# Performance work log

Measured on AMD Instinct MI355X. Metric: run time of the kernel, lower is better.

Reference implementation:

```python
import jax, jax.numpy as jnp
import numpy as np
import math

D, H, L, V, F, B, S = 1024, 16, 4, 32000, 4096, 1, 2048
HD = D // H
LN_EPS = 1e-5


def _alibi_slopes(n_heads):
    # power-of-2 case from the torch code
    start = 2.0 ** (-2.0 ** (-(math.log2(n_heads) - 3)))
    return np.array([start * (start ** i) for i in range(n_heads)], dtype=np.float32)


def setup_inputs() -> dict:
    key = jax.random.key(0)
    ks = jax.random.split(key, 10)
    sc = 0.02
    return {
        "input_ids": jax.random.randint(ks[0], (B, S), 0, V, dtype=jnp.int64 if jax.config.jax_enable_x64 else jnp.int32),
        "emb": jax.random.normal(ks[1], (V, D), jnp.float32) * sc,
        "alibi_slopes": jnp.asarray(_alibi_slopes(H)),
        "Wq": jax.random.normal(ks[2], (L, D, D), jnp.float32) * sc,
        "Wk": jax.random.normal(ks[3], (L, D, D), jnp.float32) * sc,
        "Wv": jax.random.normal(ks[4], (L, D, D), jnp.float32) * sc,
        "Wo": jax.random.normal(ks[5], (L, D, D), jnp.float32) * sc,
        "W1": jax.random.normal(ks[6], (L, F, D), jnp.float32) * sc,
        "b1": jnp.zeros((L, F), jnp.float32),
        "W2": jax.random.normal(ks[7], (L, D, F), jnp.float32) * sc,
        "b2": jnp.zeros((L, D), jnp.float32),
        "g1": jnp.ones((L, D), jnp.float32),
        "beta1": jnp.zeros((L, D), jnp.float32),
        "g2": jnp.ones((L, D), jnp.float32),
        "beta2": jnp.zeros((L, D), jnp.float32),
        "gf": jnp.ones((D,), jnp.float32),
        "bf": jnp.zeros((D,), jnp.float32),
    }


def _layernorm(x, g, b):
    m = jnp.mean(x, axis=-1, keepdims=True)
    v = jnp.var(x, axis=-1, keepdims=True)
    return (x - m) * jax.lax.rsqrt(v + LN_EPS) * g + b


def _forward(input_ids, emb, alibi_slopes, Wq, Wk, Wv, Wo, W1, b1, W2, b2,
             g1, beta1, g2, beta2, gf, bf):
    x = emb[input_ids]  # [B, S, D]
    pos = jnp.arange(S, dtype=jnp.float32)
    dist = pos[None, :] - pos[:, None]          # [S, S], entry (i, j) = j - i
    causal = dist <= 0                           # tril mask
    bias = alibi_slopes[None, :, None, None] * dist  # [1, H, S, S]
    scale = 1.0 / math.sqrt(HD)

    def layer(x, p):
        wq, wk, wv, wo, w1, bb1, w2, bb2, gg1, be1, gg2, be2 = p
        h = _layernorm(x, gg1, be1)
        q = jnp.einsum('bsd,ed->bse', h, wq).reshape(B, S, H, HD).transpose(0, 2, 1, 3)
        k = jnp.einsum('bsd,ed->bse', h, wk).reshape(B, S, H, HD).transpose(0, 2, 1, 3)
        v = jnp.einsum('bsd,ed->bse', h, wv).reshape(B, S, H, HD).transpose(0, 2, 1, 3)
        scores = jnp.einsum('bhqd,bhkd->bhqk', q, k) * scale
        scores = scores - bias
        scores = jnp.where(causal, scores, -jnp.inf)
        w = jax.nn.softmax(scores, axis=-1)
        out = jnp.einsum('bhqk,bhkd->bhqd', w, v)
        out = out.transpose(0, 2, 1, 3).reshape(B, S, D)
        out = jnp.einsum('bsd,ed->bse', out, wo)
        x = x + out
        h2 = _layernorm(x, gg2, be2)
        ff = jax.nn.gelu(jnp.einsum('bsd,fd->bsf', h2, w1) + bb1, approximate=False)
        ff = jnp.einsum('bsf,df->bsd', ff, w2) + bb2
        return x + ff, None

    params = (Wq, Wk, Wv, Wo, W1, b1, W2, b2, g1, beta1, g2, beta2)
    x, _ = jax.lax.scan(layer, x, params)
    x = _layernorm(x, gf, bf)
    logits = jnp.einsum('bsd,vd->bsv', x, emb)  # tied lm_head
    return logits


def reference(input_ids, emb, alibi_slopes, Wq, Wk, Wv, Wo, W1, b1, W2, b2,
              g1, beta1, g2, beta2, gf, bf):
    return _forward(input_ids, emb, alibi_slopes, Wq, Wk, Wv, Wo, W1, b1, W2, b2,
                    g1, beta1, g2, beta2, gf, bf)
```

## Files before the change

kernel.cpp:

```cpp
#include <hip/hip_runtime.h>
#include <hip/hip_bf16.h>

typedef unsigned int u32;
typedef unsigned short u16;
typedef __attribute__((ext_vector_type(8))) __bf16 bf16x8;
typedef __attribute__((ext_vector_type(8))) unsigned short u16x8;
typedef __attribute__((ext_vector_type(4))) float f32x4;

#define SEQ 2048

__device__ __forceinline__ float b2f(u16 u) {
  union { u32 i; float f; } x; x.i = ((u32)u) << 16; return x.f;
}
__device__ __forceinline__ u16 f2b(float f) {
  u32 u = __float_as_uint(f);
  u = (u + 0x7fffu + ((u >> 16) & 1u)) >> 16;
  return (u16)u;
}
__device__ __forceinline__ void gload_lds16(const void* g, void* l) {
  __builtin_amdgcn_global_load_lds((const __attribute__((address_space(1))) u32*)g,
                                   (__attribute__((address_space(3))) u32*)l, 16, 0, 0);
}

struct CvtArgs {
  const float* src[7];
  u16* dst[7];
  u32 beg[8];
  u32 total;
};

__global__ __launch_bounds__(256) void cvt_all(CvtArgs a)
{
  for (u32 i = blockIdx.x * 256 + threadIdx.x; i < a.total; i += gridDim.x * 256) {
    int s = 0;
#pragma unroll
    for (int k = 1; k < 7; ++k) s += (i >= a.beg[k]);
    const u32 li = i - a.beg[s];
    const float* in = a.src[s];
    const float4 f0 = ((const float4*)in)[(size_t)li * 2];
    const float4 f1 = ((const float4*)in)[(size_t)li * 2 + 1];
    union { bf16x8 b; u16x8 u; } r;
    r.b[0] = (__bf16)f0.x; r.b[1] = (__bf16)f0.y;
    r.b[2] = (__bf16)f0.z; r.b[3] = (__bf16)f0.w;
    r.b[4] = (__bf16)f1.x; r.b[5] = (__bf16)f1.y;
    r.b[6] = (__bf16)f1.z; r.b[7] = (__bf16)f1.w;
    *(u16x8*)(a.dst[s] + (size_t)li * 8) = r.u;
  }
}

template <int EPI>
__global__ __launch_bounds__(256) void gemm_bt64(
    const u16* __restrict__ A, const u16* __restrict__ Bt,
    void* __restrict__ C0, int N, int K)
{
  __shared__ u16 As[128 * 64];
  __shared__ u16 Bs[128 * 64];
  const int tid = threadIdx.x;
  const int lane = tid & 63;
  const int w = tid >> 6;
  const int wr = w >> 1;
  const int wc = w & 1;

  const int T = (int)gridDim.x;
  const int bid = (int)blockIdx.x;
  const int q8 = T >> 3, r8 = T & 7;
  const int xcd = bid & 7, base = bid >> 3;
  int swz = (xcd < r8 ? xcd * (q8 + 1) : r8 * (q8 + 1) + (xcd - r8) * q8) + base;
  const int m0 = (swz & 15) * 128;
  const int n0 = (swz >> 4) * 128;

  f32x4 acc[4][4] = {};

  const int rs = lane >> 3;
  const int gs = (lane & 7) ^ rs;
  const u16* ga0 = A + (size_t)(m0 + w * 32 + rs) * K + gs * 8;
  const u16* gb0 = Bt + (size_t)(n0 + w * 32 + rs) * K + gs * 8;
  u16* la = &As[(w * 32) * 64];
  u16* lb = &Bs[(w * 32) * 64];

  const int xg = lane & 7;
  int coff[2];
#pragma unroll
  for (int ks = 0; ks < 2; ++ks)
    coff[ks] = ((ks * 4 + (lane >> 4)) ^ xg) * 8;
  const int ra = (wr * 64 + (lane & 15)) * 64;
  const int rb = (wc * 64 + (lane & 15)) * 64;

  for (int kt = 0; kt < K; kt += 64) {
    __syncthreads();
#pragma unroll
    for (int c = 0; c < 4; ++c) {
      gload_lds16(ga0 + (size_t)c * 8 * K + kt, la + c * 8 * 64);
      gload_lds16(gb0 + (size_t)c * 8 * K + kt, lb + c * 8 * 64);
    }
    asm volatile("s_waitcnt vmcnt(0)" ::: "memory");
    __syncthreads();
#pragma unroll
    for (int ks = 0; ks < 2; ++ks) {
      bf16x8 af[4], bfr[4];
#pragma unroll
      for (int m = 0; m < 4; ++m)
        af[m] = *(const bf16x8*)&As[ra + m * 16 * 64 + coff[ks]];
#pragma unroll
      for (int n = 0; n < 4; ++n)
        bfr[n] = *(const bf16x8*)&Bs[rb + n * 16 * 64 + coff[ks]];
#pragma unroll
      for (int m = 0; m < 4; ++m)
#pragma unroll
        for (int n = 0; n < 4; ++n)
          acc[m][n] = __builtin_amdgcn_mfma_f32_16x16x32_bf16(af[m], bfr[n], acc[m][n], 0, 0, 0);
    }
  }

#pragma unroll
  for (int m = 0; m < 4; ++m) {
    const int rowb = m0 + wr * 64 + m * 16 + ((lane >> 4) << 2);
#pragma unroll
    for (int n = 0; n < 4; ++n) {
      const int col = n0 + wc * 64 + n * 16 + (lane & 15);
#pragma unroll
      for (int j = 0; j < 4; ++j)
        ((float*)C0)[(size_t)(rowb + j) * N + col] = acc[m][n][j];
    }
  }
}

template <int EPI>
__global__ __launch_bounds__(256) void gemm64(
    const u16* __restrict__ A, const u16* __restrict__ B0,
    const u16* __restrict__ B1, const u16* __restrict__ B2,
    void* __restrict__ C0, void* __restrict__ C1, void* __restrict__ C2,
    const float* __restrict__ bias, int N, int K)
{
  __shared__ u16 As[64 * 64];
  __shared__ u16 Bs[128 * 64];
  const int tid = threadIdx.x;
  const int lane = tid & 63;
  const int w = tid >> 6;
  const int wr = w >> 1;
  const int wc = w & 1;

  const int T = (int)gridDim.x;
  const int bid = (int)blockIdx.x;
  const int q8 = T >> 3, r8 = T & 7;
  const int xcd = bid & 7, base = bid >> 3;
  int swz = (xcd < r8 ? xcd * (q8 + 1) : r8 * (q8 + 1) + (xcd - r8) * q8) + base;
  int which = 0;
  if (EPI == 1) which = swz >> 8;
  const u16* Bt = (which == 0) ? B0 : (which == 1) ? B1 : B2;
  const int m0 = (swz & 31) * 64;
  const int n0 = (EPI == 1 ? ((swz >> 5) & 7) : (swz >> 5)) * 128;

  const int kchunk = K / (int)gridDim.z;
  const int kbeg = (int)blockIdx.z * kchunk;
  const int kend = kbeg + kchunk;

  f32x4 acc[2][4] = {};

  const int rs = lane >> 3;
  const int gs = (lane & 7) ^ rs;
  const u16* ga0 = A + (size_t)(m0 + w * 16 + rs) * K + gs * 8;
  const u16* gb0 = Bt + (size_t)(n0 + w * 32 + rs) * K + gs * 8;
  u16* la = &As[(w * 16) * 64];
  u16* lb = &Bs[(w * 32) * 64];

  const int xg = lane & 7;
  int coff[2];
#pragma unroll
  for (int ks = 0; ks < 2; ++ks)
    coff[ks] = ((ks * 4 + (lane >> 4)) ^ xg) * 8;
  const int ra = (wr * 32 + (lane & 15)) * 64;
  const int rb = (wc * 64 + (lane & 15)) * 64;

  for (int kt = kbeg; kt < kend; kt += 64) {
    __syncthreads();
#pragma unroll
    for (int c = 0; c < 2; ++c)
      gload_lds16(ga0 + (size_t)c * 8 * K + kt, la + c * 8 * 64);
#pragma unroll
    for (int c = 0; c < 4; ++c)
      gload_lds16(gb0 + (size_t)c * 8 * K + kt, lb + c * 8 * 64);
    asm volatile("s_waitcnt vmcnt(0)" ::: "memory");
    __syncthreads();
#pragma unroll
    for (int ks = 0; ks < 2; ++ks) {
      bf16x8 af[2], bfr[4];
#pragma unroll
      for (int m = 0; m < 2; ++m)
        af[m] = *(const bf16x8*)&As[ra + m * 16 * 64 + coff[ks]];
#pragma unroll
      for (int n = 0; n < 4; ++n)
        bfr[n] = *(const bf16x8*)&Bs[rb + n * 16 * 64 + coff[ks]];
#pragma unroll
      for (int m = 0; m < 2; ++m)
#pragma unroll
        for (int n = 0; n < 4; ++n)
          acc[m][n] = __builtin_amdgcn_mfma_f32_16x16x32_bf16(af[m], bfr[n], acc[m][n], 0, 0, 0);
    }
  }

#pragma unroll
  for (int m = 0; m < 2; ++m) {
    const int rowb = m0 + wr * 32 + m * 16 + ((lane >> 4) << 2);
#pragma unroll
    for (int n = 0; n < 4; ++n) {
      const int col = n0 + wc * 64 + n * 16 + (lane & 15);
#pragma unroll
      for (int j = 0; j < 4; ++j) {
        const int r = rowb + j;
        float v = acc[m][n][j];
        if (EPI == 1) {
          u16* outp = (u16*)((which == 0) ? C0 : (which == 1) ? C1 : C2);
          outp[((size_t)(col >> 6) * SEQ + r) * 64 + (col & 63)] = f2b(v);
        } else if (EPI == 2) {
          float xx = v + bias[col];
          float ge = 0.5f * xx * (1.0f + erff(xx * 0.70710678118654752f));
          ((u16*)C0)[(size_t)r * N + col] = f2b(ge);
        } else {
          float xx = v;
          if (bias != nullptr && blockIdx.z == 0) xx += bias[col];
          atomicAdd(&((float*)C0)[(size_t)r * N + col], xx);
        }
      }
    }
  }
}

__global__ __launch_bounds__(256) void gemm_f32b(
    const u16* __restrict__ A, const float* __restrict__ Bt,
    float* __restrict__ C0, int N, int K)
{
  __shared__ u16 As[128 * 32];
  __shared__ u16 Bs[128 * 32];
  const int tid = threadIdx.x;
  const int lane = tid & 63;
  const int w = tid >> 6;
  const int wr = w >> 1;
  const int wc = w & 1;

  const int T = (int)gridDim.x;
  const int bid = (int)blockIdx.x;
  const int q8 = T >> 3, r8 = T & 7;
  const int xcd = bid & 7, base = bid >> 3;
  int swz = (xcd < r8 ? xcd * (q8 + 1) : r8 * (q8 + 1) + (xcd - r8) * q8) + base;
  const int m0 = (swz & 15) * 128;
  const int n0 = (swz >> 4) * 128;

  f32x4 acc[4][4] = {};
  const u16* ga0 = A + (size_t)(m0 + w * 32 + (lane >> 2)) * K + (lane & 3) * 8;
  u16* la = &As[(w * 32) * 32];
  const float* gb32 = Bt + (size_t)(n0 + (tid >> 1)) * K + (tid & 1) * 16;
  u16* lbw = &Bs[(tid >> 1) * 32 + (tid & 1) * 16];

  for (int kt = 0; kt < K; kt += 32) {
    __syncthreads();
    gload_lds16(ga0 + kt, la);
    gload_lds16(ga0 + kt + 16 * K, la + 16 * 32);
    {
      const float4 f0 = *(const float4*)(gb32 + kt);
      const float4 f1 = *(const float4*)(gb32 + kt + 4);
      const float4 f2 = *(const float4*)(gb32 + kt + 8);
      const float4 f3 = *(const float4*)(gb32 + kt + 12);
      union { bf16x8 b; u16x8 u; } lo, hi;
      lo.b[0] = (__bf16)f0.x; lo.b[1] = (__bf16)f0.y;
      lo.b[2] = (__bf16)f0.z; lo.b[3] = (__bf16)f0.w;
      lo.b[4] = (__bf16)f1.x; lo.b[5] = (__bf16)f1.y;
      lo.b[6] = (__bf16)f1.z; lo.b[7] = (__bf16)f1.w;
      hi.b[0] = (__bf16)f2.x; hi.b[1] = (__bf16)f2.y;
      hi.b[2] = (__bf16)f2.z; hi.b[3] = (__bf16)f2.w;
      hi.b[4] = (__bf16)f3.x; hi.b[5] = (__bf16)f3.y;
      hi.b[6] = (__bf16)f3.z; hi.b[7] = (__bf16)f3.w;
      *(u16x8*)lbw = lo.u;
      *(u16x8*)(lbw + 8) = hi.u;
    }
    asm volatile("s_waitcnt vmcnt(0)" ::: "memory");
    __syncthreads();
    bf16x8 af[4], bfr[4];
#pragma unroll
    for (int m = 0; m < 4; ++m)
      af[m] = *(const bf16x8*)&As[(wr * 64 + m * 16 + (lane & 15)) * 32 + (lane >> 4) * 8];
#pragma unroll
    for (int n = 0; n < 4; ++n)
      bfr[n] = *(const bf16x8*)&Bs[(wc * 64 + n * 16 + (lane & 15)) * 32 + (lane >> 4) * 8];
#pragma unroll
    for (int m = 0; m < 4; ++m)
#pragma unroll
      for (int n = 0; n < 4; ++n)
        acc[m][n] = __builtin_amdgcn_mfma_f32_16x16x32_bf16(af[m], bfr[n], acc[m][n], 0, 0, 0);
  }

#pragma unroll
  for (int m = 0; m < 4; ++m) {
    const int rowb = m0 + wr * 64 + m * 16 + ((lane >> 4) << 2);
#pragma unroll
    for (int n = 0; n < 4; ++n) {
      const int col = n0 + wc * 64 + n * 16 + (lane & 15);
#pragma unroll
      for (int j = 0; j < 4; ++j)
        C0[(size_t)(rowb + j) * N + col] = acc[m][n][j];
    }
  }
}

__global__ __launch_bounds__(256) void ln_kernel(const float* __restrict__ x,
    const float* __restrict__ g, const float* __restrict__ b, u16* __restrict__ out)
{
  const int row = blockIdx.x;
  const int tid = threadIdx.x;
  const float4 v = ((const float4*)(x + (size_t)row * 1024))[tid];
  float s = v.x + v.y + v.z + v.w;
  float sq = v.x * v.x + v.y * v.y + v.z * v.z + v.w * v.w;
#pragma unroll
  for (int o = 1; o < 64; o <<= 1) { s += __shfl_xor(s, o); sq += __shfl_xor(sq, o); }
  __shared__ float ss[4], ssq[4];
  if ((tid & 63) == 0) { ss[tid >> 6] = s; ssq[tid >> 6] = sq; }
  __syncthreads();
  s = ss[0] + ss[1] + ss[2] + ss[3];
  sq = ssq[0] + ssq[1] + ssq[2] + ssq[3];
  const float mean = s * (1.0f / 1024.0f);
  const float var = sq * (1.0f / 1024.0f) - mean * mean;
  const float rstd = rsqrtf(var + 1e-5f);
  const int c = tid * 4;
  u16* o4 = out + (size_t)row * 1024 + c;
  const float4 gg = ((const float4*)g)[tid];
  const float4 bb = ((const float4*)b)[tid];
  o4[0] = f2b((v.x - mean) * rstd * gg.x + bb.x);
  o4[1] = f2b((v.y - mean) * rstd * gg.y + bb.y);
  o4[2] = f2b((v.z - mean) * rstd * gg.z + bb.z);
  o4[3] = f2b((v.w - mean) * rstd * gg.w + bb.w);
}

__global__ __launch_bounds__(256) void gather_kernel(const int* __restrict__ ids,
    const float* __restrict__ emb, float* __restrict__ x)
{
  const int srow = blockIdx.x;
  const int tid = threadIdx.x;
  const int id = ids[srow];
  ((float4*)(x + (size_t)srow * 1024))[tid] =
      ((const float4*)(emb + (size_t)id * 1024))[tid];
}

__global__ __launch_bounds__(256) void attn_kernel(
    const u16* __restrict__ q, const u16* __restrict__ k, const u16* __restrict__ v,
    const float* __restrict__ slopes, u16* __restrict__ out)
{
  const int bid = (int)blockIdx.x;
  const int swz = (bid & 7) * 32 + (bid >> 3);
  const int h = swz >> 4;
  const int q0 = (swz & 15) * 128;
  const int tid = threadIdx.x;
  const int lane = tid & 63;
  const int w = tid >> 6;
  const float slope = slopes[h];

  __shared__ u16 Ks[2][64 * 32];
  __shared__ u16 Vt[64][72];
  __shared__ u16 Pl[4][32][72];

  const u16* qb = q + ((size_t)h * SEQ + q0 + w * 32) * 64;
  bf16x8 qf[2][2];
#pragma unroll
  for (int m = 0; m < 2; ++m)
#pragma unroll
    for (int kk = 0; kk < 2; ++kk)
      qf[m][kk] = *(const bf16x8*)(qb + (m * 16 + (lane & 15)) * 64 + kk * 32 + (lane >> 4) * 8);

  f32x4 o_acc[2][4] = {};
  float mrun[2][4], lrun[2][4];
#pragma unroll
  for (int m = 0; m < 2; ++m)
#pragma unroll
    for (int j = 0; j < 4; ++j) { mrun[m][j] = -1e30f; lrun[m][j] = 0.0f; }

  const int ntiles = (q0 >> 6) + 2;
  const int wmaxrow = q0 + w * 32 + 31;

  const int kkp = w >> 1, halfp = w & 1;
  const u16* gk0 = k + ((size_t)h * SEQ + halfp * 32 + (lane >> 2)) * 64 + kkp * 32 + (lane & 3) * 8;
  u16* lk = &Ks[kkp][(halfp * 32) * 32];
  const u16* gv0 = v + ((size_t)h * SEQ + lane) * 64 + w * 16;

  for (int t = 0; t < ntiles; ++t) {
    const int j0 = t << 6;
    __syncthreads();
    gload_lds16(gk0 + (size_t)j0 * 64, lk);
    gload_lds16(gk0 + (size_t)(j0 + 16) * 64, lk + 16 * 32);
    {
      const u16* gvp = gv0 + (size_t)j0 * 64;
      u16x8 v0 = *(const u16x8*)gvp;
      u16x8 v1 = *(const u16x8*)(gvp + 8);
      const int d0 = w * 16;
#pragma unroll
      for (int i = 0; i < 8; ++i) Vt[d0 + i][lane] = v0[i];
#pragma unroll
      for (int i = 0; i < 8; ++i) Vt[d0 + 8 + i][lane] = v1[i];
    }
    asm volatile("s_waitcnt vmcnt(0)" ::: "memory");
    __syncthreads();

    if (wmaxrow >= j0) {
      f32x4 s[2][4] = {};
      __builtin_amdgcn_s_setprio(1);
#pragma unroll
      for (int kk = 0; kk < 2; ++kk) {
        bf16x8 kf[4];
#pragma unroll
        for (int n = 0; n < 4; ++n)
          kf[n] = *(const bf16x8*)&Ks[kk][(n * 16 + (lane & 15)) * 32 + (lane >> 4) * 8];
#pragma unroll
        for (int m = 0; m < 2; ++m)
#pragma unroll
          for (int n = 0; n < 4; ++n)
            s[m][n] = __builtin_amdgcn_mfma_f32_16x16x32_bf16(qf[m][kk], kf[n], s[m][n], 0, 0, 0);
      }
      __builtin_amdgcn_s_setprio(0);
      const int rq = q0 + w * 32 + ((lane >> 4) << 2);
      const int ck = j0 + (lane & 15);
#pragma unroll
      for (int m = 0; m < 2; ++m) {
#pragma unroll
        for (int j = 0; j < 4; ++j) {
          const int qi = rq + m * 16 + j;
          float mx = -1e30f;
#pragma unroll
          for (int n = 0; n < 4; ++n) {
            const int kj = ck + n * 16;
            float val = s[m][n][j] * 0.125f - slope * (float)(kj - qi);
            val = (kj <= qi) ? val : -1e30f;
            s[m][n][j] = val;
            mx = fmaxf(mx, val);
          }
#pragma unroll
          for (int o = 1; o < 16; o <<= 1) mx = fmaxf(mx, __shfl_xor(mx, o));
          const float mnew = fmaxf(mrun[m][j], mx);
          const float alpha = __expf(mrun[m][j] - mnew);
          mrun[m][j] = mnew;
          float rs = 0.0f;
          const int prow = m * 16 + ((lane >> 4) << 2) + j;
#pragma unroll
          for (int n = 0; n < 4; ++n) {
            const float p = __expf(s[m][n][j] - mnew);
            rs += p;
            Pl[w][prow][n * 16 + (lane & 15)] = f2b(p);
          }
#pragma unroll
          for (int o = 1; o < 16; o <<= 1) rs += __shfl_xor(rs, o);
          lrun[m][j] = lrun[m][j] * alpha + rs;
#pragma unroll
          for (int n = 0; n < 4; ++n) o_acc[m][n][j] *= alpha;
        }
      }
      __builtin_amdgcn_s_setprio(1);
#pragma unroll
      for (int kk = 0; kk < 2; ++kk) {
        bf16x8 pf[2], vf[4];
#pragma unroll
        for (int m = 0; m < 2; ++m)
          pf[m] = *(const bf16x8*)&Pl[w][m * 16 + (lane & 15)][kk * 32 + (lane >> 4) * 8];
#pragma unroll
        for (int n = 0; n < 4; ++n)
          vf[n] = *(const bf16x8*)&Vt[n * 16 + (lane & 15)][kk * 32 + (lane >> 4) * 8];
#pragma unroll
        for (int m = 0; m < 2; ++m)
#pragma unroll
          for (int n = 0; n < 4; ++n)
            o_acc[m][n] = __builtin_amdgcn_mfma_f32_16x16x32_bf16(pf[m], vf[n], o_acc[m][n], 0, 0, 0);
      }
      __builtin_amdgcn_s_setprio(0);
    }
  }

#pragma unroll
  for (int m = 0; m < 2; ++m) {
    const int sbase = q0 + w * 32 + m * 16 + ((lane >> 4) << 2);
#pragma unroll
    for (int n = 0; n < 4; ++n) {
      const int d = h * 64 + n * 16 + (lane & 15);
#pragma unroll
      for (int j = 0; j < 4; ++j)
        out[(size_t)(sbase + j) * 1024 + d] = f2b(o_acc[m][n][j] / lrun[m][j]);
    }
  }
}

extern "C" void kernel_launch(void* const* d_in, const int* in_sizes, int n_in,
                              void* d_out, int out_size, void* d_ws, size_t ws_size,
                              hipStream_t stream)
{
  (void)in_sizes; (void)n_in; (void)out_size;
  const int* ids = (const int*)d_in[0];
  const float* emb = (const float*)d_in[1];
  const float* slopes = (const float*)d_in[2];
  const float* Wq = (const float*)d_in[3];
  const float* Wk = (const float*)d_in[4];
  const float* Wv = (const float*)d_in[5];
  const float* Wo = (const float*)d_in[6];
  const float* W1 = (const float*)d_in[7];
  const float* b1 = (const float*)d_in[8];
  const float* W2 = (const float*)d_in[9];
  const float* b2 = (const float*)d_in[10];
  const float* g1 = (const float*)d_in[11];
  const float* be1 = (const float*)d_in[12];
  const float* g2 = (const float*)d_in[13];
  const float* be2 = (const float*)d_in[14];
  const float* gf = (const float*)d_in[15];
  const float* bfin = (const float*)d_in[16];

  char* ob = (char*)d_out;
  float* x   = (float*)ob;
  u16* qb    = (u16*)(ob + (size_t)( 8u << 20));
  u16* kb    = (u16*)(ob + (size_t)(12u << 20));
  u16* vb    = (u16*)(ob + (size_t)(16u << 20));
  u16* attn  = (u16*)(ob + (size_t)(20u << 20));
  u16* ff    = (u16*)(ob + (size_t)(24u << 20));
  u16* Wq_b  = (u16*)(ob + (size_t)( 40u << 20));
  u16* Wk_b  = (u16*)(ob + (size_t)( 48u << 20));
  u16* Wv_b  = (u16*)(ob + (size_t)( 56u << 20));
  u16* Wo_b  = (u16*)(ob + (size_t)( 64u << 20));
  u16* W1_b  = (u16*)(ob + (size_t)( 72u << 20));
  u16* W2_b  = (u16*)(ob + (size_t)(104u << 20));
  u16* h     = (u16*)d_ws;
  const size_t emb_b_need = (size_t)(4u << 20) + (size_t)32000 * 1024 * 2;
  const bool emb_fits = ws_size >= emb_b_need;
  u16* emb_b = (u16*)((char*)d_ws + (4u << 20));
  float* logits = (float*)d_out;

  {
    CvtArgs a;
    const u32 wsz = 4 * 1024 * 1024 / 8;
    const u32 fsz = 16 * 1024 * 1024 / 8;
    const u32 esz = 32000 * 1024 / 8;
    a.src[0] = Wq; a.dst[0] = Wq_b;
    a.src[1] = Wk; a.dst[1] = Wk_b;
    a.src[2] = Wv; a.dst[2] = Wv_b;
    a.src[3] = Wo; a.dst[3] = Wo_b;
    a.src[4] = W1; a.dst[4] = W1_b;
    a.src[5] = W2; a.dst[5] = W2_b;
    a.src[6] = emb; a.dst[6] = emb_b;
    a.beg[0] = 0;
    a.beg[1] = wsz;      a.beg[2] = 2 * wsz;  a.beg[3] = 3 * wsz;
    a.beg[4] = 4 * wsz;  a.beg[5] = 4 * wsz + fsz;  a.beg[6] = 4 * wsz + 2 * fsz;
    a.beg[7] = a.beg[6] + esz;
    a.total = emb_fits ? a.beg[7] : a.beg[6];
    cvt_all<<<2048, 256, 0, stream>>>(a);
  }

  gather_kernel<<<2048, 256, 0, stream>>>(ids, emb, x);

  for (int l = 0; l < 4; ++l) {
    const size_t wo = (size_t)l * 1024 * 1024;
    const size_t wf = (size_t)l * 4096 * 1024;
    ln_kernel<<<2048, 256, 0, stream>>>(x, g1 + l * 1024, be1 + l * 1024, h);
    gemm64<1><<<dim3(768, 1, 1), 256, 0, stream>>>(h, Wq_b + wo, Wk_b + wo, Wv_b + wo,
        qb, kb, vb, nullptr, 1024, 1024);
    attn_kernel<<<dim3(256, 1, 1), 256, 0, stream>>>(qb, kb, vb, slopes, attn);
    gemm64<3><<<dim3(256, 1, 2), 256, 0, stream>>>(attn, Wo_b + wo, nullptr, nullptr,
        x, nullptr, nullptr, nullptr, 1024, 1024);
    ln_kernel<<<2048, 256, 0, stream>>>(x, g2 + l * 1024, be2 + l * 1024, h);
    gemm64<2><<<dim3(1024, 1, 1), 256, 0, stream>>>(h, W1_b + wf, nullptr, nullptr,
        ff, nullptr, nullptr, b1 + l * 4096, 4096, 1024);
    gemm64<3><<<dim3(256, 1, 2), 256, 0, stream>>>(ff, W2_b + wf, nullptr, nullptr,
        x, nullptr, nullptr, b2 + l * 1024, 1024, 4096);
  }
  ln_kernel<<<2048, 256, 0, stream>>>(x, gf, bfin, h);
  if (emb_fits) {
    gemm_bt64<0><<<dim3(4000, 1, 1), 256, 0, stream>>>(h, emb_b, logits, 32000, 1024);
  } else {
    gemm_f32b<<<dim3(4000, 1, 1), 256, 0, stream>>>(h, emb, logits, 32000, 1024);
  }
}
```

Before: 1.353 ms.

## Replace lm_head GEMM with 256x256 double-buffered 8-wave kernel

Swaps the 128x128 single-buffered logits GEMM for a 256x256-tile kernel with 512 threads, double-buffered LDS and next-tile global-to-LDS loads interleaved with MFMA phases, plus setprio around the MFMA bursts. The aim is higher arithmetic intensity per tile and hiding global load latency behind compute in the largest GEMM (2048x32000x1024). The cost is 128KB of LDS per block and more accumulator registers, which limits occupancy, and a grid of 1000 blocks that leaves a tail imbalance across CUs.

```diff
diff --git a/kernel.cpp b/kernel.cpp
--- a/kernel.cpp
+++ b/kernel.cpp
@@ -48,81 +48,109 @@
   }
 }
 
-template <int EPI>
-__global__ __launch_bounds__(256) void gemm_bt64(
+__global__ __launch_bounds__(512, 2) void gemm256(
     const u16* __restrict__ A, const u16* __restrict__ Bt,
-    void* __restrict__ C0, int N, int K)
-{
-  __shared__ u16 As[128 * 64];
-  __shared__ u16 Bs[128 * 64];
+    float* __restrict__ C, int N, int K)
+{
+  __shared__ u16 As[2][256 * 64];
+  __shared__ u16 Bs[2][256 * 64];
   const int tid = threadIdx.x;
   const int lane = tid & 63;
-  const int w = tid >> 6;
-  const int wr = w >> 1;
-  const int wc = w & 1;
+  const int wid = tid >> 6;
+  const int wr = wid >> 2;
+  const int wc = wid & 3;
 
   const int T = (int)gridDim.x;
   const int bid = (int)blockIdx.x;
   const int q8 = T >> 3, r8 = T & 7;
   const int xcd = bid & 7, base = bid >> 3;
-  int swz = (xcd < r8 ? xcd * (q8 + 1) : r8 * (q8 + 1) + (xcd - r8) * q8) + base;
-  const int m0 = (swz & 15) * 128;
-  const int n0 = (swz >> 4) * 128;
-
-  f32x4 acc[4][4] = {};
-
-  const int rs = lane >> 3;
-  const int gs = (lane & 7) ^ rs;
-  const u16* ga0 = A + (size_t)(m0 + w * 32 + rs) * K + gs * 8;
-  const u16* gb0 = Bt + (size_t)(n0 + w * 32 + rs) * K + gs * 8;
-  u16* la = &As[(w * 32) * 64];
-  u16* lb = &Bs[(w * 32) * 64];
-
-  const int xg = lane & 7;
-  int coff[2];
-#pragma unroll
-  for (int ks = 0; ks < 2; ++ks)
-    coff[ks] = ((ks * 4 + (lane >> 4)) ^ xg) * 8;
-  const int ra = (wr * 64 + (lane & 15)) * 64;
-  const int rb = (wc * 64 + (lane & 15)) * 64;
-
-  for (int kt = 0; kt < K; kt += 64) {
-    __syncthreads();
-#pragma unroll
-    for (int c = 0; c < 4; ++c) {
-      gload_lds16(ga0 + (size_t)c * 8 * K + kt, la + c * 8 * 64);
-      gload_lds16(gb0 + (size_t)c * 8 * K + kt, lb + c * 8 * 64);
-    }
-    asm volatile("s_waitcnt vmcnt(0)" ::: "memory");
-    __syncthreads();
-#pragma unroll
-    for (int ks = 0; ks < 2; ++ks) {
-      bf16x8 af[4], bfr[4];
-#pragma unroll
-      for (int m = 0; m < 4; ++m)
-        af[m] = *(const bf16x8*)&As[ra + m * 16 * 64 + coff[ks]];
-#pragma unroll
-      for (int n = 0; n < 4; ++n)
-        bfr[n] = *(const bf16x8*)&Bs[rb + n * 16 * 64 + coff[ks]];
-#pragma unroll
-      for (int m = 0; m < 4; ++m)
-#pragma unroll
-        for (int n = 0; n < 4; ++n)
-          acc[m][n] = __builtin_amdgcn_mfma_f32_16x16x32_bf16(af[m], bfr[n], acc[m][n], 0, 0, 0);
-    }
-  }
-
-#pragma unroll
-  for (int m = 0; m < 4; ++m) {
-    const int rowb = m0 + wr * 64 + m * 16 + ((lane >> 4) << 2);
-#pragma unroll
-    for (int n = 0; n < 4; ++n) {
-      const int col = n0 + wc * 64 + n * 16 + (lane & 15);
+  const int swz = (xcd < r8 ? xcd * (q8 + 1) : r8 * (q8 + 1) + (xcd - r8) * q8) + base;
+  const int m0 = (swz & 7) * 256;
+  const int n0 = (swz >> 3) * 256;
+
+  f32x4 acc[8][4] = {};
+
+  const int srow = tid >> 3;
+  const int sgr = (tid & 7) ^ (srow & 7);
+  const u16* gA = A + (size_t)(m0 + srow) * K + sgr * 8;
+  const u16* gB = Bt + (size_t)(n0 + srow) * K + sgr * 8;
+  const int dwave = wid * 512;
+
+  const int co0 = (((lane >> 4)) ^ (lane & 7)) * 8;
+  const int co1 = (((lane >> 4) + 4) ^ (lane & 7)) * 8;
+  const int raA = (wr * 128 + (lane & 15)) * 64;
+  const int raB = (wc * 64 + (lane & 15)) * 64;
+
+#pragma unroll
+  for (int c = 0; c < 4; ++c) {
+    gload_lds16(gA + (size_t)(c * 64) * K, &As[0][c * 4096 + dwave]);
+    gload_lds16(gB + (size_t)(c * 64) * K, &Bs[0][c * 4096 + dwave]);
+  }
+  asm volatile("s_waitcnt vmcnt(0)" ::: "memory");
+  __syncthreads();
+
+  const int nk = K >> 6;
+#pragma unroll 2
+  for (int t = 0; t < nk; ++t) {
+    const int cb = t & 1;
+    const int sb = cb ^ 1;
+    const u16* Acur = &As[cb][0];
+    const u16* Bcur = &Bs[cb][0];
+    u16* Anxt = &As[sb][0];
+    u16* Bnxt = &Bs[sb][0];
+    const size_t ktn = (size_t)(t + 1) * 64;
+    const bool stg = (t + 1 < nk);
+    bf16x8 bf[4][2];
+#pragma unroll
+    for (int p = 0; p < 4; ++p) {
+      bf16x8 af[2][2];
+#pragma unroll
+      for (int mm = 0; mm < 2; ++mm) {
+        const int ro = raA + (p * 32 + mm * 16) * 64;
+        af[mm][0] = *(const bf16x8*)&Acur[ro + co0];
+        af[mm][1] = *(const bf16x8*)&Acur[ro + co1];
+      }
+      if (p == 0) {
+#pragma unroll
+        for (int n = 0; n < 4; ++n) {
+          const int ro = raB + n * 16 * 64;
+          bf[n][0] = *(const bf16x8*)&Bcur[ro + co0];
+          bf[n][1] = *(const bf16x8*)&Bcur[ro + co1];
+        }
+      }
+      if (stg) {
+        if (p < 2) {
+          gload_lds16(gA + (size_t)((p * 2 + 0) * 64) * K + ktn, Anxt + (p * 2 + 0) * 4096 + dwave);
+          gload_lds16(gA + (size_t)((p * 2 + 1) * 64) * K + ktn, Anxt + (p * 2 + 1) * 4096 + dwave);
+        } else {
+          gload_lds16(gB + (size_t)(((p - 2) * 2 + 0) * 64) * K + ktn, Bnxt + ((p - 2) * 2 + 0) * 4096 + dwave);
+          gload_lds16(gB + (size_t)(((p - 2) * 2 + 1) * 64) * K + ktn, Bnxt + ((p - 2) * 2 + 1) * 4096 + dwave);
+        }
+      }
+      __syncthreads();
+      __builtin_amdgcn_s_setprio(1);
+#pragma unroll
+      for (int mm = 0; mm < 2; ++mm)
+#pragma unroll
+        for (int n = 0; n < 4; ++n) {
+          acc[p * 2 + mm][n] = __builtin_amdgcn_mfma_f32_16x16x32_bf16(af[mm][0], bf[n][0], acc[p * 2 + mm][n], 0, 0, 0);
+          acc[p * 2 + mm][n] = __builtin_amdgcn_mfma_f32_16x16x32_bf16(af[mm][1], bf[n][1], acc[p * 2 + mm][n], 0, 0, 0);
+        }
+      __builtin_amdgcn_s_setprio(0);
+      if (p == 3) asm volatile("s_waitcnt vmcnt(0)" ::: "memory");
+      __syncthreads();
+    }
+  }
+
+  const int crow = m0 + wr * 128 + ((lane >> 4) << 2);
+  const int ccol = n0 + wc * 64 + (lane & 15);
+#pragma unroll
+  for (int m = 0; m < 8; ++m)
+#pragma unroll
+    for (int n = 0; n < 4; ++n)
 #pragma unroll
       for (int j = 0; j < 4; ++j)
-        ((float*)C0)[(size_t)(rowb + j) * N + col] = acc[m][n][j];
-    }
-  }
+        C[(size_t)(crow + m * 16 + j) * N + ccol + n * 16] = acc[m][n][j];
 }
 
 template <int EPI>
@@ -564,7 +592,7 @@
   }
   ln_kernel<<<2048, 256, 0, stream>>>(x, gf, bfin, h);
   if (emb_fits) {
-    gemm_bt64<0><<<dim3(4000, 1, 1), 256, 0, stream>>>(h, emb_b, logits, 32000, 1024);
+    gemm256<<<dim3(1000, 1, 1), 512, 0, stream>>>(h, emb_b, logits, 32000, 1024);
   } else {
     gemm_f32b<<<dim3(4000, 1, 1), 256, 0, stream>>>(h, emb, logits, 32000, 1024);
   }
```

New measurement: 1.385 ms. 2.4% more time.
